# Optimization experiments

Measured on AMD Instinct MI355X. Metric: run time of the kernel, lower is better.

## Reference

```python
import jax, jax.numpy as jnp
import numpy as np

B, L, H, N = 8, 2048, 512, 64  # batch, seq_len, d_model, SSM state size


def setup_inputs() -> dict:
    key = jax.random.key(0)
    ks = jax.random.split(key, 10)
    x = jax.random.normal(ks[0], (B, L, H), jnp.float32)
    # S4D-style parameters (diagonal SSM, S4D-Lin init)
    log_dt = jnp.log(1e-3) + jax.random.uniform(ks[1], (H,), jnp.float32) * (jnp.log(1e-1) - jnp.log(1e-3))
    A_re = -0.5 * jnp.ones((H, N), jnp.float32)
    A_im = jnp.tile(np.pi * jnp.arange(N, dtype=np.float32), (H, 1))
    C_re = jax.random.normal(ks[2], (H, N), jnp.float32) * (0.5 ** 0.5)
    C_im = jax.random.normal(ks[3], (H, N), jnp.float32) * (0.5 ** 0.5)
    D_skip = jax.random.normal(ks[4], (H,), jnp.float32)
    # S4 output linear (GLU): d_model -> 2*d_model, then gated
    W_out = jax.random.normal(ks[5], (2 * H, H), jnp.float32) / np.sqrt(H)
    b_out = jnp.zeros((2 * H,), jnp.float32)
    # LayerNorms
    g1 = jnp.ones((H,), jnp.float32); beta1 = jnp.zeros((H,), jnp.float32)
    g2 = jnp.ones((H,), jnp.float32); beta2 = jnp.zeros((H,), jnp.float32)
    # 1x1 conv FFN (kernel_size=1 => pointwise linear), d_ff = d_model
    W1 = jax.random.normal(ks[6], (H, H), jnp.float32) / np.sqrt(H)
    bc1 = jnp.zeros((H,), jnp.float32)
    W2 = jax.random.normal(ks[7], (H, H), jnp.float32) / np.sqrt(H)
    bc2 = jnp.zeros((H,), jnp.float32)
    return dict(x=x, log_dt=log_dt, A_re=A_re, A_im=A_im, C_re=C_re, C_im=C_im,
                D_skip=D_skip, W_out=W_out, b_out=b_out, g1=g1, beta1=beta1,
                g2=g2, beta2=beta2, W1=W1, bc1=bc1, W2=W2, bc2=bc2)


def _layer_norm(x, g, b):
    mu = jnp.mean(x, axis=-1, keepdims=True)
    var = jnp.mean((x - mu) ** 2, axis=-1, keepdims=True)
    return (x - mu) / jnp.sqrt(var + 1e-5) * g + b


def _s4(x, log_dt, A_re, A_im, C_re, C_im, D_skip, W_out, b_out):
    # x: (B, L, H) channels-last (transposed=False)
    Lx = x.shape[1]
    dt = jnp.exp(log_dt)                       # (H,)
    A = A_re + 1j * A_im                       # (H, N) diagonal state matrix
    dtA = A * dt[:, None]
    # ZOH discretization of C: Ct = C * (exp(dt*A) - 1) / A
    Ct = (C_re + 1j * C_im) * ((jnp.exp(dtA) - 1.0) / A)
    # Vandermonde kernel: K[h, l] = 2 Re sum_n Ct[h,n] exp(dt*A[h,n]*l)
    l = jnp.arange(Lx, dtype=jnp.float32)
    K = 2.0 * jnp.real(jnp.einsum('hn,hnl->hl', Ct, jnp.exp(dtA[:, :, None] * l)))
    # FFT long convolution (linear conv via zero-padded circular conv)
    u = jnp.swapaxes(x, 1, 2)                  # (B, H, L)
    n = 2 * Lx
    y = jnp.fft.irfft(jnp.fft.rfft(u, n) * jnp.fft.rfft(K, n)[None], n)[..., :Lx]
    y = y + D_skip[None, :, None] * u          # skip connection D*u
    y = jax.nn.gelu(y)                         # S4 default activation
    # output linear + GLU (S4 default postact)
    z = jnp.einsum('bhl,fh->bfl', y, W_out) + b_out[None, :, None]
    a, g = jnp.split(z, 2, axis=1)
    y = a * jax.nn.sigmoid(g)
    return jnp.swapaxes(y, 1, 2)               # (B, L, H)


def reference(x, log_dt, A_re, A_im, C_re, C_im, D_skip, W_out, b_out,
              g1, beta1, g2, beta2, W1, bc1, W2, bc2):
    new_x = _s4(x, log_dt, A_re, A_im, C_re, C_im, D_skip, W_out, b_out)
    x = x + new_x
    x = _layer_norm(x, g1, beta1)
    # FFN via 1x1 convs (pointwise linears); dropout is identity in eval
    y = jax.nn.relu(jnp.einsum('blh,fh->blf', x, W1) + bc1)
    y = jnp.einsum('blf,hf->blh', y, W2) + bc2
    return _layer_norm(x + y, g2, beta2)
```

## Files before the change

### kernel.cpp

```cpp
#include <hip/hip_runtime.h>
#include <cstddef>
#include <cstdint>

#define B_DIM 8
#define L_DIM 2048
#define H_DIM 512
#define N_DIM 64
#define HN (H_DIM * N_DIM)
#define BLH (B_DIM * L_DIM * H_DIM)
#define M_DIM (B_DIM * L_DIM)

typedef unsigned short u16;
typedef short bf16x8 __attribute__((ext_vector_type(8)));
typedef float floatx4 __attribute__((ext_vector_type(4)));

__device__ __forceinline__ float sigmoidf_(float v) {
    return 1.0f / (1.0f + __expf(-v));
}

__device__ __forceinline__ float gelu_tanh_(float x) {
    float x3 = x * x * x;
    float z = 0.7978845608028654f * fmaf(0.044715f, x3, x);
    float e = __expf(-2.0f * fabsf(z));
    float th = (1.0f - e) / (1.0f + e);
    th = copysignf(th, z);
    return 0.5f * x * (1.0f + th);
}

__device__ __forceinline__ u16 f2b(float f) {
    unsigned u = __float_as_uint(f);
    unsigned r = (u + 0x7fffu + ((u >> 16) & 1u)) >> 16;
    return (u16)r;
}
__device__ __forceinline__ float b2f(u16 u) {
    return __uint_as_float(((unsigned)u) << 16);
}
__device__ __forceinline__ void unpack2(unsigned u, float& a, float& b) {
    a = __uint_as_float(u << 16);
    b = __uint_as_float(u & 0xffff0000u);
}
__device__ __forceinline__ unsigned pack2(float a, float b) {
    return (unsigned)f2b(a) | ((unsigned)f2b(b) << 16);
}

__device__ __forceinline__ void csq(float& r, float& i) {
    float nr = r * r - i * i;
    i = 2.0f * r * i;
    r = nr;
}

__global__ __launch_bounds__(256) void cast_kernel(
    const float* __restrict__ src, u16* __restrict__ dst)
{
    int i = blockIdx.x * 256 + threadIdx.x;
    float4 v = *(const float4*)(src + (size_t)i * 4);
    uint2 p;
    p.x = pack2(v.x, v.y);
    p.y = pack2(v.z, v.w);
    *(uint2*)(dst + (size_t)i * 4) = p;
}

__global__ __launch_bounds__(256) void precompute_kernel(
    const float* __restrict__ log_dt, const float* __restrict__ A_re,
    const float* __restrict__ A_im, const float* __restrict__ C_re,
    const float* __restrict__ C_im, float* __restrict__ P)
{
    int i = blockIdx.x * 256 + threadIdx.x;
    if (i >= HN) return;
    int h = i >> 6;
    float dt = expf(log_dt[h]);
    float Ar = A_re[i], Ai = A_im[i];
    float ar = dt * Ar, ai = dt * Ai;
    float e = expf(ar);
    float wr = e * cosf(ai);
    float wi = e * sinf(ai);
    float em1r = wr - 1.0f, em1i = wi;
    float inv = 1.0f / fmaf(Ar, Ar, Ai * Ai);
    float qr = fmaf(em1r, Ar, em1i * Ai) * inv;
    float qi = fmaf(em1i, Ar, -(em1r * Ai)) * inv;
    float Cr = C_re[i], Ci = C_im[i];
    float ctr = Cr * qr - Ci * qi;
    float cti = Cr * qi + Ci * qr;
    P[i]          = wr;
    P[HN + i]     = wi;
    P[2 * HN + i] = 2.0f * ctr;
    P[3 * HN + i] = 2.0f * cti;
}

__global__ __launch_bounds__(256) void ktab_kernel(
    const float* __restrict__ P, float* __restrict__ Ktab)
{
    int wv = threadIdx.x >> 6, lane = threadIdx.x & 63;
    int h = blockIdx.x * 4 + wv;
    int pidx = (h << 6) + lane;
    float wr = P[pidx], wi = P[HN + pidx];
    float c2r = P[2 * HN + pidx], c2i = P[3 * HN + pidx];
    float pr = 1.0f, pi = 0.0f;
    for (int tau = 0; tau < 64; ++tau) {
        float term = c2r * pr - c2i * pi;
        #pragma unroll
        for (int m = 32; m > 0; m >>= 1) term += __shfl_xor(term, m, 64);
        if (lane == 0) Ktab[(h << 6) + tau] = term;
        float nr = pr * wr - pi * wi, ni = pr * wi + pi * wr;
        pr = nr; pi = ni;
    }
}

__global__ __launch_bounds__(256) void toepfill_kernel(
    const float* __restrict__ Ktab, u16* __restrict__ Toep_bf)
{
    int idx = blockIdx.x * 256 + threadIdx.x;
    int h = idx >> 12;
    int rem = idx & 4095;
    int tt = rem >> 6, j = rem & 63;
    u16 v = 0;
    if (j <= tt) v = f2b(Ktab[(h << 6) + (tt - j)]);
    Toep_bf[idx] = v;
}

__global__ __launch_bounds__(256) void xtrans_kernel(
    const float* __restrict__ x, u16* __restrict__ XT)
{
    __shared__ float tile[32][33];
    int b  = blockIdx.z;
    int l0 = blockIdx.x * 32;
    int h0 = blockIdx.y * 32;
    int tx = threadIdx.x & 31;
    int ty = threadIdx.x >> 5;
    #pragma unroll
    for (int r = 0; r < 4; ++r)
        tile[ty + r * 8][tx] = x[((size_t)b * L_DIM + l0 + ty + r * 8) * H_DIM + h0 + tx];
    __syncthreads();
    #pragma unroll
    for (int r = 0; r < 4; ++r)
        XT[((size_t)b * H_DIM + h0 + ty + r * 8) * L_DIM + l0 + tx] = f2b(tile[tx][ty + r * 8]);
}

__global__ __launch_bounds__(256) void ssm_chunk_kernel(
    const u16* __restrict__ XT, const float* __restrict__ P,
    const u16* __restrict__ Toep_bf, const float* __restrict__ D_skip,
    u16* __restrict__ YT)
{
    __shared__ u16 U[128 * 72];
    __shared__ u16 S[128 * 136];
    __shared__ u16 EVT[13312];
    u16* E  = EVT;
    u16* Tp = EVT;
    u16* V  = EVT + 4608;

    const int h    = blockIdx.x;
    const int b0   = blockIdx.y * 4;
    const int t    = threadIdx.x;
    const int lane = t & 63;
    const int wv   = t >> 6;
    const int lm   = lane & 15, lq = lane >> 4;

    const int pidx = (h << 6) + lane;
    const float wr  = P[pidx],          wi  = P[HN + pidx];
    const float c2r = P[2 * HN + pidx], c2i = P[3 * HN + pidx];

    #pragma unroll
    for (int r = 0; r < 4; ++r) {
        int idx = t + r * 256;
        int row = idx >> 3, ch = idx & 7;
        const u16* gp = XT + (((size_t)(b0 + (row >> 5)) * H_DIM + h) << 11)
                           + ((row & 31) << 6) + (ch << 3);
        *(uint4*)&U[row * 72 + ch * 8] = *(const uint4*)gp;
    }

    float bwr, bwi;
    {
        float g16r = wr, g16i = wi;
        csq(g16r, g16i); csq(g16r, g16i); csq(g16r, g16i); csq(g16r, g16i);
        if (wv == 0)      { bwr = 1.0f; bwi = 0.0f; }
        else if (wv == 1) { bwr = g16r; bwi = g16i; }
        else if (wv == 2) { bwr = g16r; bwi = g16i; csq(bwr, bwi); }
        else {
            float g32r = g16r, g32i = g16i; csq(g32r, g32i);
            bwr = g32r * g16r - g32i * g16i;
            bwi = g32r * g16i + g32i * g16r;
        }
    }

    {
        float pr = bwr, pi = bwi;
        #pragma unroll
        for (int jk = 0; jk < 16; ++jk) {
            int k = (wv << 4) + jk;
            int j = 63 - k;
            E[(2 * lane) * 72 + j]     = f2b(pr);
            E[(2 * lane + 1) * 72 + j] = f2b(pi);
            float nr = pr * wr - pi * wi, ni = pr * wi + pi * wr;
            pr = nr; pi = ni;
        }
    }
    __syncthreads();

    {
        const int wm = wv >> 1, wn = wv & 1;
        floatx4 acc[4][4] = {};
        #pragma unroll
        for (int ks = 0; ks < 2; ++ks) {
            bf16x8 af[4], bfv[4];
            #pragma unroll
            for (int i = 0; i < 4; ++i)
                af[i] = *(const bf16x8*)&E[(wm * 64 + i * 16 + lm) * 72 + ks * 32 + lq * 8];
            #pragma unroll
            for (int j = 0; j < 4; ++j)
                bfv[j] = *(const bf16x8*)&U[(wn * 64 + j * 16 + lm) * 72 + ks * 32 + lq * 8];
            #pragma unroll
            for (int i = 0; i < 4; ++i) {
                #pragma unroll
                for (int j = 0; j < 4; ++j)
                    acc[i][j] = __builtin_amdgcn_mfma_f32_16x16x32_bf16(af[i], bfv[j], acc[i][j], 0, 0, 0);
            }
        }
        #pragma unroll
        for (int i = 0; i < 4; ++i) {
            #pragma unroll
            for (int j = 0; j < 4; ++j) {
                int ncol = wn * 64 + j * 16 + lm;
                int m0   = wm * 64 + i * 16 + lq * 4;
                u16 pk[4];
                #pragma unroll
                for (int r = 0; r < 4; ++r) pk[r] = f2b(acc[i][j][r]);
                *(uint2*)&S[ncol * 136 + m0] = *(uint2*)pk;
            }
        }
    }
    __syncthreads();

    {
        float pr = bwr, pi = bwi;
        {
            float nr = pr * wr - pi * wi, ni = pr * wi + pi * wr;
            pr = nr; pi = ni;
        }
        #pragma unroll
        for (int jk = 1; jk <= 16; ++jk) {
            int tr = (wv << 4) + jk - 1;
            float qr = c2r * pr - c2i * pi;
            float qi = c2r * pi + c2i * pr;
            V[tr * 136 + 2 * lane]     = f2b(qr);
            V[tr * 136 + 2 * lane + 1] = f2b(-qi);
            float nr = pr * wr - pi * wi, ni = pr * wi + pi * wr;
            pr = nr; pi = ni;
        }
        #pragma unroll
        for (int r = 0; r < 2; ++r) {
            int idx = t + r * 256;
            int row = idx >> 3, ch = idx & 7;
            *(uint4*)&Tp[row * 72 + ch * 8] =
                *(const uint4*)&Toep_bf[((size_t)h << 12) + (row << 6) + (ch << 3)];
        }
        float wTr = wr, wTi = wi;
        csq(wTr, wTi); csq(wTr, wTi); csq(wTr, wTi);
        csq(wTr, wTi); csq(wTr, wTi); csq(wTr, wTi);
        float Sr = 0.0f, Si = 0.0f;
        const int n2 = lane * 2;
        for (int c = 0; c < 32; ++c) {
            int base = (wv * 32 + c) * 136 + n2;
            unsigned lv = *(unsigned*)&S[base];
            float lr, li;
            unpack2(lv, lr, li);
            *(unsigned*)&S[base] = pack2(Sr, Si);
            float nSr = wTr * Sr - wTi * Si + lr;
            Si = wTr * Si + wTi * Sr + li;
            Sr = nSr;
        }
    }
    __syncthreads();

    {
        const float Dh = D_skip[h];
        floatx4 acc[4][2] = {};
        #pragma unroll
        for (int ks = 0; ks < 6; ++ks) {
            bf16x8 af[4], bfv[2];
            if (ks < 2) {
                #pragma unroll
                for (int i = 0; i < 4; ++i)
                    af[i] = *(const bf16x8*)&Tp[(i * 16 + lm) * 72 + ks * 32 + lq * 8];
                #pragma unroll
                for (int j = 0; j < 2; ++j)
                    bfv[j] = *(const bf16x8*)&U[(wv * 32 + j * 16 + lm) * 72 + ks * 32 + lq * 8];
            } else {
                #pragma unroll
                for (int i = 0; i < 4; ++i)
                    af[i] = *(const bf16x8*)&V[(i * 16 + lm) * 136 + (ks - 2) * 32 + lq * 8];
                #pragma unroll
                for (int j = 0; j < 2; ++j)
                    bfv[j] = *(const bf16x8*)&S[(wv * 32 + j * 16 + lm) * 136 + (ks - 2) * 32 + lq * 8];
            }
            #pragma unroll
            for (int i = 0; i < 4; ++i) {
                #pragma unroll
                for (int j = 0; j < 2; ++j)
                    acc[i][j] = __builtin_amdgcn_mfma_f32_16x16x32_bf16(af[i], bfv[j], acc[i][j], 0, 0, 0);
            }
        }
        #pragma unroll
        for (int j = 0; j < 2; ++j) {
            int ncol = wv * 32 + j * 16 + lm;
            int bloc = ncol >> 5, c = ncol & 31;
            size_t gbase = (((size_t)(b0 + bloc) * H_DIM + h) << 11) + (c << 6);
            #pragma unroll
            for (int i = 0; i < 4; ++i) {
                int t0 = i * 16 + lq * 4;
                u16 upk[4];
                *(uint2*)upk = *(const uint2*)&U[ncol * 72 + t0];
                u16 opk[4];
                #pragma unroll
                for (int r = 0; r < 4; ++r) {
                    float uvv = b2f(upk[r]);
                    float yv = gelu_tanh_(fmaf(Dh, uvv, acc[i][j][r]));
                    opk[r] = f2b(yv);
                }
                *(uint2*)&YT[gbase + t0] = *(uint2*)opk;
            }
        }
    }
}

__global__ __launch_bounds__(256) void ytrans_kernel(
    const u16* __restrict__ YT, u16* __restrict__ Y)
{
    __shared__ u16 tile[32][33];
    int b  = blockIdx.z;
    int l0 = blockIdx.x * 32;
    int h0 = blockIdx.y * 32;
    int tx = threadIdx.x & 31;
    int ty = threadIdx.x >> 5;
    #pragma unroll
    for (int r = 0; r < 4; ++r)
        tile[ty + r * 8][tx] = YT[((size_t)b * H_DIM + h0 + ty + r * 8) * L_DIM + l0 + tx];
    __syncthreads();
    #pragma unroll
    for (int r = 0; r < 4; ++r)
        Y[((size_t)b * L_DIM + l0 + ty + r * 8) * H_DIM + h0 + tx] = tile[tx][ty + r * 8];
}

__device__ __forceinline__ void stage_tile_128x32(
    const u16* __restrict__ g, u16* lds, int row0, int k0)
{
    const int t = threadIdx.x;
    #pragma unroll
    for (int r = 0; r < 2; ++r) {
        int row = (t >> 2) + r * 64;
        int col = (t & 3) * 8;
        const u16* gp = g + (size_t)(row0 + row) * 512 + k0 + col;
        __builtin_amdgcn_global_load_lds(
            (const __attribute__((address_space(1))) unsigned int*)gp,
            (__attribute__((address_space(3))) unsigned int*)(lds + (size_t)t * 8 + (size_t)r * 2048),
            16, 0, 0);
    }
}

__global__ __launch_bounds__(256) void gemm1_glu_kernel(
    const u16* __restrict__ A, const u16* __restrict__ Wo,
    const float* __restrict__ bo, const float* __restrict__ x,
    u16* __restrict__ out)
{
    __shared__ u16 As[2][128 * 32];
    __shared__ u16 Ba[2][128 * 32];
    __shared__ u16 Bg[2][128 * 32];
    const int t    = threadIdx.x;
    const int lane = t & 63;
    const int wv   = t >> 6;
    const int wm   = wv >> 1, wn = wv & 1;
    const int lm   = lane & 15, lq = lane >> 4;
    const int m0   = blockIdx.x * 128, n0 = blockIdx.y * 128;
    floatx4 accA[4][4] = {};
    floatx4 accG[4][4] = {};

    stage_tile_128x32(A, As[0], m0, 0);
    stage_tile_128x32(Wo, Ba[0], n0, 0);
    stage_tile_128x32(Wo, Bg[0], 512 + n0, 0);
    __syncthreads();

    int cur = 0;
    for (int k0 = 32; k0 < 512; k0 += 32) {
        const int nx = cur ^ 1;
        stage_tile_128x32(A, As[nx], m0, k0);
        stage_tile_128x32(Wo, Ba[nx], n0, k0);
        stage_tile_128x32(Wo, Bg[nx], 512 + n0, k0);

        bf16x8 af[4], ba[4], bg[4];
        #pragma unroll
        for (int i = 0; i < 4; ++i)
            af[i] = *(const bf16x8*)&As[cur][(wm * 64 + i * 16 + lm) * 32 + lq * 8];
        #pragma unroll
        for (int j = 0; j < 4; ++j) {
            ba[j] = *(const bf16x8*)&Ba[cur][(wn * 64 + j * 16 + lm) * 32 + lq * 8];
            bg[j] = *(const bf16x8*)&Bg[cur][(wn * 64 + j * 16 + lm) * 32 + lq * 8];
        }
        #pragma unroll
        for (int i = 0; i < 4; ++i) {
            #pragma unroll
            for (int j = 0; j < 4; ++j) {
                accA[i][j] = __builtin_amdgcn_mfma_f32_16x16x32_bf16(af[i], ba[j], accA[i][j], 0, 0, 0);
                accG[i][j] = __builtin_amdgcn_mfma_f32_16x16x32_bf16(af[i], bg[j], accG[i][j], 0, 0, 0);
            }
        }
        __syncthreads();
        cur = nx;
    }
    {
        bf16x8 af[4], ba[4], bg[4];
        #pragma unroll
        for (int i = 0; i < 4; ++i)
            af[i] = *(const bf16x8*)&As[cur][(wm * 64 + i * 16 + lm) * 32 + lq * 8];
        #pragma unroll
        for (int j = 0; j < 4; ++j) {
            ba[j] = *(const bf16x8*)&Ba[cur][(wn * 64 + j * 16 + lm) * 32 + lq * 8];
            bg[j] = *(const bf16x8*)&Bg[cur][(wn * 64 + j * 16 + lm) * 32 + lq * 8];
        }
        #pragma unroll
        for (int i = 0; i < 4; ++i) {
            #pragma unroll
            for (int j = 0; j < 4; ++j) {
                accA[i][j] = __builtin_amdgcn_mfma_f32_16x16x32_bf16(af[i], ba[j], accA[i][j], 0, 0, 0);
                accG[i][j] = __builtin_amdgcn_mfma_f32_16x16x32_bf16(af[i], bg[j], accG[i][j], 0, 0, 0);
            }
        }
    }
    #pragma unroll
    for (int j = 0; j < 4; ++j) {
        int n = n0 + wn * 64 + j * 16 + lm;
        float bav = bo[n], bgv = bo[512 + n];
        #pragma unroll
        for (int i = 0; i < 4; ++i) {
            #pragma unroll
            for (int r = 0; r < 4; ++r) {
                int m = m0 + wm * 64 + i * 16 + lq * 4 + r;
                float av = accA[i][j][r] + bav;
                float gv = accG[i][j][r] + bgv;
                float xv = x[(size_t)m * 512 + n];
                out[(size_t)m * 512 + n] = f2b(fmaf(av, sigmoidf_(gv), xv));
            }
        }
    }
}

template<int EPI>
__global__ __launch_bounds__(256) void gemm_bt_bf_kernel(
    const u16* __restrict__ A, const u16* __restrict__ Bw,
    const float* __restrict__ bias, u16* __restrict__ C)
{
    __shared__ u16 As[2][128 * 32];
    __shared__ u16 Bs[2][128 * 32];
    const int t    = threadIdx.x;
    const int lane = t & 63;
    const int wv   = t >> 6;
    const int wm   = wv >> 1, wn = wv & 1;
    const int lm   = lane & 15, lq = lane >> 4;
    const int m0   = blockIdx.x * 128, n0 = blockIdx.y * 128;
    floatx4 acc[4][4] = {};

    stage_tile_128x32(A, As[0], m0, 0);
    stage_tile_128x32(Bw, Bs[0], n0, 0);
    __syncthreads();

    int cur = 0;
    for (int k0 = 32; k0 < 512; k0 += 32) {
        const int nx = cur ^ 1;
        stage_tile_128x32(A, As[nx], m0, k0);
        stage_tile_128x32(Bw, Bs[nx], n0, k0);

        bf16x8 af[4], bfr[4];
        #pragma unroll
        for (int i = 0; i < 4; ++i)
            af[i] = *(const bf16x8*)&As[cur][(wm * 64 + i * 16 + lm) * 32 + lq * 8];
        #pragma unroll
        for (int j = 0; j < 4; ++j)
            bfr[j] = *(const bf16x8*)&Bs[cur][(wn * 64 + j * 16 + lm) * 32 + lq * 8];
        #pragma unroll
        for (int i = 0; i < 4; ++i) {
            #pragma unroll
            for (int j = 0; j < 4; ++j)
                acc[i][j] = __builtin_amdgcn_mfma_f32_16x16x32_bf16(af[i], bfr[j], acc[i][j], 0, 0, 0);
        }
        __syncthreads();
        cur = nx;
    }
    {
        bf16x8 af[4], bfr[4];
        #pragma unroll
        for (int i = 0; i < 4; ++i)
            af[i] = *(const bf16x8*)&As[cur][(wm * 64 + i * 16 + lm) * 32 + lq * 8];
        #pragma unroll
        for (int j = 0; j < 4; ++j)
            bfr[j] = *(const bf16x8*)&Bs[cur][(wn * 64 + j * 16 + lm) * 32 + lq * 8];
        #pragma unroll
        for (int i = 0; i < 4; ++i) {
            #pragma unroll
            for (int j = 0; j < 4; ++j)
                acc[i][j] = __builtin_amdgcn_mfma_f32_16x16x32_bf16(af[i], bfr[j], acc[i][j], 0, 0, 0);
        }
    }
    #pragma unroll
    for (int j = 0; j < 4; ++j) {
        int n = n0 + wn * 64 + j * 16 + lm;
        float bv = bias[n];
        #pragma unroll
        for (int i = 0; i < 4; ++i) {
            #pragma unroll
            for (int r = 0; r < 4; ++r) {
                int m = m0 + wm * 64 + i * 16 + lq * 4 + r;
                float v = acc[i][j][r] + bv;
                if (EPI == 1) v = fmaxf(v, 0.0f);
                C[(size_t)m * 512 + n] = f2b(v);
            }
        }
    }
}

template<bool HASRES, bool F32OUT>
__global__ __launch_bounds__(256) void ln_bf_kernel(
    const u16* __restrict__ in, const u16* __restrict__ res,
    const float* __restrict__ gamma, const float* __restrict__ beta,
    u16* __restrict__ outb, float* __restrict__ outf)
{
    int w    = threadIdx.x >> 6;
    int lane = threadIdx.x & 63;
    size_t row  = (size_t)blockIdx.x * 4 + w;
    size_t base = row * 512 + lane * 8;
    uint4 raw = *(const uint4*)(in + base);
    float v[8];
    unpack2(raw.x, v[0], v[1]); unpack2(raw.y, v[2], v[3]);
    unpack2(raw.z, v[4], v[5]); unpack2(raw.w, v[6], v[7]);
    if (HASRES) {
        uint4 rr = *(const uint4*)(res + base);
        float rv[8];
        unpack2(rr.x, rv[0], rv[1]); unpack2(rr.y, rv[2], rv[3]);
        unpack2(rr.z, rv[4], rv[5]); unpack2(rr.w, rv[6], rv[7]);
        #pragma unroll
        for (int i = 0; i < 8; ++i) v[i] += rv[i];
    }
    float s = 0.0f, sq = 0.0f;
    #pragma unroll
    for (int i = 0; i < 8; ++i) { s += v[i]; sq = fmaf(v[i], v[i], sq); }
    #pragma unroll
    for (int m = 32; m > 0; m >>= 1) {
        s  += __shfl_xor(s, m, 64);
        sq += __shfl_xor(sq, m, 64);
    }
    float mu  = s * (1.0f / 512.0f);
    float var = sq * (1.0f / 512.0f) - mu * mu;
    float rs  = rsqrtf(var + 1e-5f);
    float g[8], bt[8];
    *(float4*)&g[0]  = *(const float4*)(gamma + lane * 8);
    *(float4*)&g[4]  = *(const float4*)(gamma + lane * 8 + 4);
    *(float4*)&bt[0] = *(const float4*)(beta + lane * 8);
    *(float4*)&bt[4] = *(const float4*)(beta + lane * 8 + 4);
    float o[8];
    #pragma unroll
    for (int i = 0; i < 8; ++i)
        o[i] = fmaf((v[i] - mu) * rs, g[i], bt[i]);
    if (F32OUT) {
        *(float4*)(outf + base)     = *(float4*)&o[0];
        *(float4*)(outf + base + 4) = *(float4*)&o[4];
    } else {
        uint4 p;
        p.x = pack2(o[0], o[1]); p.y = pack2(o[2], o[3]);
        p.z = pack2(o[4], o[5]); p.w = pack2(o[6], o[7]);
        *(uint4*)(outb + base) = p;
    }
}

extern "C" void kernel_launch(void* const* d_in, const int* in_sizes, int n_in,
                              void* d_out, int out_size, void* d_ws, size_t ws_size,
                              hipStream_t stream)
{
    (void)in_sizes; (void)n_in; (void)out_size; (void)ws_size;
    const float* x      = (const float*)d_in[0];
    const float* log_dt = (const float*)d_in[1];
    const float* A_re   = (const float*)d_in[2];
    const float* A_im   = (const float*)d_in[3];
    const float* C_re   = (const float*)d_in[4];
    const float* C_im   = (const float*)d_in[5];
    const float* D_skip = (const float*)d_in[6];
    const float* W_out  = (const float*)d_in[7];
    const float* b_out  = (const float*)d_in[8];
    const float* g1     = (const float*)d_in[9];
    const float* beta1  = (const float*)d_in[10];
    const float* g2     = (const float*)d_in[11];
    const float* beta2  = (const float*)d_in[12];
    const float* W1     = (const float*)d_in[13];
    const float* bc1    = (const float*)d_in[14];
    const float* W2     = (const float*)d_in[15];
    const float* bc2    = (const float*)d_in[16];
    float* out = (float*)d_out;

    char*  wsb    = (char*)d_ws;
    float* P      = (float*)wsb;
    float* Ktab   = (float*)(wsb + 4 * HN * 4);
    u16*   Toep   = (u16*)(wsb + 4 * HN * 4 + 512 * 64 * 4);
    u16*   Wobf   = Toep + 512 * 4096;
    u16*   W1bf   = Wobf + 1024 * 512;
    u16*   W2bf   = W1bf + 512 * 512;
    u16*   r1     = W2bf + 512 * 512;
    u16*   r2     = r1 + BLH;
    u16*   r3     = r2 + BLH;

    cast_kernel<<<512, 256, 0, stream>>>(W_out, Wobf);
    cast_kernel<<<256, 256, 0, stream>>>(W1, W1bf);
    cast_kernel<<<256, 256, 0, stream>>>(W2, W2bf);
    precompute_kernel<<<HN / 256, 256, 0, stream>>>(log_dt, A_re, A_im, C_re, C_im, P);
    ktab_kernel<<<128, 256, 0, stream>>>(P, Ktab);
    toepfill_kernel<<<8192, 256, 0, stream>>>(Ktab, Toep);
    xtrans_kernel<<<dim3(L_DIM / 32, H_DIM / 32, B_DIM), 256, 0, stream>>>(x, r1);
    ssm_chunk_kernel<<<dim3(H_DIM, 2), 256, 0, stream>>>(r1, P, Toep, D_skip, r2);
    ytrans_kernel<<<dim3(L_DIM / 32, H_DIM / 32, B_DIM), 256, 0, stream>>>(r2, r3);
    gemm1_glu_kernel<<<dim3(M_DIM / 128, 4), 256, 0, stream>>>(r3, Wobf, b_out, x, r2);
    ln_bf_kernel<false, false><<<M_DIM / 4, 256, 0, stream>>>(r2, nullptr, g1, beta1, r1, nullptr);
    gemm_bt_bf_kernel<1><<<dim3(M_DIM / 128, 4), 256, 0, stream>>>(r1, W1bf, bc1, r3);
    gemm_bt_bf_kernel<0><<<dim3(M_DIM / 128, 4), 256, 0, stream>>>(r3, W2bf, bc2, r2);
    ln_bf_kernel<true, true><<<M_DIM / 4, 256, 0, stream>>>(r2, r1, g2, beta2, nullptr, out);
}
```

Baseline: 253.8 us.

## Use 512-thread GEMM blocks with XOR-swizzled LDS tiles

The three bf16 GEMM kernels now run 8 waves per block instead of 4. Each wave computes a 64x32 sub-tile instead of 64x64, which halves accumulator registers per wave and roughly doubles the waves available to hide latency. Tile staging changes to one 16-byte global-to-LDS load per thread, with an XOR swizzle on the source column. Fragment reads apply the matching swizzle to avoid LDS bank conflicts. In exchange, the A fragments are reloaded by twice as many waves, which adds LDS read traffic per MFMA.

```diff
diff --git a/kernel.cpp b/kernel.cpp
--- a/kernel.cpp
+++ b/kernel.cpp
@@ -340,23 +340,20 @@
         Y[((size_t)b * L_DIM + l0 + ty + r * 8) * H_DIM + h0 + tx] = tile[tx][ty + r * 8];
 }
 
-__device__ __forceinline__ void stage_tile_128x32(
+__device__ __forceinline__ void stage_tile_512(
     const u16* __restrict__ g, u16* lds, int row0, int k0)
 {
     const int t = threadIdx.x;
-    #pragma unroll
-    for (int r = 0; r < 2; ++r) {
-        int row = (t >> 2) + r * 64;
-        int col = (t & 3) * 8;
-        const u16* gp = g + (size_t)(row0 + row) * 512 + k0 + col;
-        __builtin_amdgcn_global_load_lds(
-            (const __attribute__((address_space(1))) unsigned int*)gp,
-            (__attribute__((address_space(3))) unsigned int*)(lds + (size_t)t * 8 + (size_t)r * 2048),
-            16, 0, 0);
-    }
-}
-
-__global__ __launch_bounds__(256) void gemm1_glu_kernel(
+    const int row  = t >> 2;
+    const int csrc = (t & 3) ^ ((t >> 3) & 3);
+    const u16* gp = g + (size_t)(row0 + row) * 512 + k0 + csrc * 8;
+    __builtin_amdgcn_global_load_lds(
+        (const __attribute__((address_space(1))) unsigned int*)gp,
+        (__attribute__((address_space(3))) unsigned int*)(lds + (size_t)t * 8),
+        16, 0, 0);
+}
+
+__global__ __launch_bounds__(512) void gemm1_glu_kernel(
     const u16* __restrict__ A, const u16* __restrict__ Wo,
     const float* __restrict__ bo, const float* __restrict__ x,
     u16* __restrict__ out)
@@ -367,37 +364,38 @@
     const int t    = threadIdx.x;
     const int lane = t & 63;
     const int wv   = t >> 6;
-    const int wm   = wv >> 1, wn = wv & 1;
+    const int wm   = wv >> 2, wn = wv & 3;
     const int lm   = lane & 15, lq = lane >> 4;
+    const int sw   = (lq ^ ((lm >> 1) & 3)) * 8;
     const int m0   = blockIdx.x * 128, n0 = blockIdx.y * 128;
-    floatx4 accA[4][4] = {};
-    floatx4 accG[4][4] = {};
-
-    stage_tile_128x32(A, As[0], m0, 0);
-    stage_tile_128x32(Wo, Ba[0], n0, 0);
-    stage_tile_128x32(Wo, Bg[0], 512 + n0, 0);
+    floatx4 accA[4][2] = {};
+    floatx4 accG[4][2] = {};
+
+    stage_tile_512(A, As[0], m0, 0);
+    stage_tile_512(Wo, Ba[0], n0, 0);
+    stage_tile_512(Wo, Bg[0], 512 + n0, 0);
     __syncthreads();
 
     int cur = 0;
     for (int k0 = 32; k0 < 512; k0 += 32) {
         const int nx = cur ^ 1;
-        stage_tile_128x32(A, As[nx], m0, k0);
-        stage_tile_128x32(Wo, Ba[nx], n0, k0);
-        stage_tile_128x32(Wo, Bg[nx], 512 + n0, k0);
-
-        bf16x8 af[4], ba[4], bg[4];
+        stage_tile_512(A, As[nx], m0, k0);
+        stage_tile_512(Wo, Ba[nx], n0, k0);
+        stage_tile_512(Wo, Bg[nx], 512 + n0, k0);
+
+        bf16x8 af[4], ba[2], bg[2];
         #pragma unroll
         for (int i = 0; i < 4; ++i)
-            af[i] = *(const bf16x8*)&As[cur][(wm * 64 + i * 16 + lm) * 32 + lq * 8];
-        #pragma unroll
-        for (int j = 0; j < 4; ++j) {
-            ba[j] = *(const bf16x8*)&Ba[cur][(wn * 64 + j * 16 + lm) * 32 + lq * 8];
-            bg[j] = *(const bf16x8*)&Bg[cur][(wn * 64 + j * 16 + lm) * 32 + lq * 8];
+            af[i] = *(const bf16x8*)&As[cur][(wm * 64 + i * 16 + lm) * 32 + sw];
+        #pragma unroll
+        for (int j = 0; j < 2; ++j) {
+            ba[j] = *(const bf16x8*)&Ba[cur][(wn * 32 + j * 16 + lm) * 32 + sw];
+            bg[j] = *(const bf16x8*)&Bg[cur][(wn * 32 + j * 16 + lm) * 32 + sw];
         }
         #pragma unroll
         for (int i = 0; i < 4; ++i) {
             #pragma unroll
-            for (int j = 0; j < 4; ++j) {
+            for (int j = 0; j < 2; ++j) {
                 accA[i][j] = __builtin_amdgcn_mfma_f32_16x16x32_bf16(af[i], ba[j], accA[i][j], 0, 0, 0);
                 accG[i][j] = __builtin_amdgcn_mfma_f32_16x16x32_bf16(af[i], bg[j], accG[i][j], 0, 0, 0);
             }
@@ -406,27 +404,27 @@
         cur = nx;
     }
     {
-        bf16x8 af[4], ba[4], bg[4];
+        bf16x8 af[4], ba[2], bg[2];
         #pragma unroll
         for (int i = 0; i < 4; ++i)
-            af[i] = *(const bf16x8*)&As[cur][(wm * 64 + i * 16 + lm) * 32 + lq * 8];
-        #pragma unroll
-        for (int j = 0; j < 4; ++j) {
-            ba[j] = *(const bf16x8*)&Ba[cur][(wn * 64 + j * 16 + lm) * 32 + lq * 8];
-            bg[j] = *(const bf16x8*)&Bg[cur][(wn * 64 + j * 16 + lm) * 32 + lq * 8];
+            af[i] = *(const bf16x8*)&As[cur][(wm * 64 + i * 16 + lm) * 32 + sw];
+        #pragma unroll
+        for (int j = 0; j < 2; ++j) {
+            ba[j] = *(const bf16x8*)&Ba[cur][(wn * 32 + j * 16 + lm) * 32 + sw];
+            bg[j] = *(const bf16x8*)&Bg[cur][(wn * 32 + j * 16 + lm) * 32 + sw];
         }
         #pragma unroll
         for (int i = 0; i < 4; ++i) {
             #pragma unroll
-            for (int j = 0; j < 4; ++j) {
+            for (int j = 0; j < 2; ++j) {
                 accA[i][j] = __builtin_amdgcn_mfma_f32_16x16x32_bf16(af[i], ba[j], accA[i][j], 0, 0, 0);
                 accG[i][j] = __builtin_amdgcn_mfma_f32_16x16x32_bf16(af[i], bg[j], accG[i][j], 0, 0, 0);
             }
         }
     }
     #pragma unroll
-    for (int j = 0; j < 4; ++j) {
-        int n = n0 + wn * 64 + j * 16 + lm;
+    for (int j = 0; j < 2; ++j) {
+        int n = n0 + wn * 32 + j * 16 + lm;
         float bav = bo[n], bgv = bo[512 + n];
         #pragma unroll
         for (int i = 0; i < 4; ++i) {
@@ -443,7 +441,7 @@
 }
 
 template<int EPI>
-__global__ __launch_bounds__(256) void gemm_bt_bf_kernel(
+__global__ __launch_bounds__(512) void gemm_bt_bf_kernel(
     const u16* __restrict__ A, const u16* __restrict__ Bw,
     const float* __restrict__ bias, u16* __restrict__ C)
 {
@@ -452,55 +450,56 @@
     const int t    = threadIdx.x;
     const int lane = t & 63;
     const int wv   = t >> 6;
-    const int wm   = wv >> 1, wn = wv & 1;
+    const int wm   = wv >> 2, wn = wv & 3;
     const int lm   = lane & 15, lq = lane >> 4;
+    const int sw   = (lq ^ ((lm >> 1) & 3)) * 8;
     const int m0   = blockIdx.x * 128, n0 = blockIdx.y * 128;
-    floatx4 acc[4][4] = {};
-
-    stage_tile_128x32(A, As[0], m0, 0);
-    stage_tile_128x32(Bw, Bs[0], n0, 0);
+    floatx4 acc[4][2] = {};
+
+    stage_tile_512(A, As[0], m0, 0);
+    stage_tile_512(Bw, Bs[0], n0, 0);
     __syncthreads();
 
     int cur = 0;
     for (int k0 = 32; k0 < 512; k0 += 32) {
         const int nx = cur ^ 1;
-        stage_tile_128x32(A, As[nx], m0, k0);
-        stage_tile_128x32(Bw, Bs[nx], n0, k0);
-
-        bf16x8 af[4], bfr[4];
+        stage_tile_512(A, As[nx], m0, k0);
+        stage_tile_512(Bw, Bs[nx], n0, k0);
+
+        bf16x8 af[4], bfr[2];
         #pragma unroll
         for (int i = 0; i < 4; ++i)
-            af[i] = *(const bf16x8*)&As[cur][(wm * 64 + i * 16 + lm) * 32 + lq * 8];
-        #pragma unroll
-        for (int j = 0; j < 4; ++j)
-            bfr[j] = *(const bf16x8*)&Bs[cur][(wn * 64 + j * 16 + lm) * 32 + lq * 8];
+            af[i] = *(const bf16x8*)&As[cur][(wm * 64 + i * 16 + lm) * 32 + sw];
+        #pragma unroll
+        for (int j = 0; j < 2; ++j)
+            bfr[j] = *(const bf16x8*)&Bs[cur][(wn * 32 + j * 16 + lm) * 32 + sw];
         #pragma unroll
         for (int i = 0; i < 4; ++i) {
             #pragma unroll
-            for (int j = 0; j < 4; ++j)
+            for (int j = 0; j < 2; ++j)
                 acc[i][j] = __builtin_amdgcn_mfma_f32_16x16x32_bf16(af[i], bfr[j], acc[i][j], 0, 0, 0);
         }
         __syncthreads();
         cur = nx;
     }
     {
-        bf16x8 af[4], bfr[4];
+        bf16x8 af[4], bfr[2];
         #pragma unroll
         for (int i = 0; i < 4; ++i)
-            af[i] = *(const bf16x8*)&As[cur][(wm * 64 + i * 16 + lm) * 32 + lq * 8];
-        #pragma unroll
-        for (int j = 0; j < 4; ++j)
-            bfr[j] = *(const bf16x8*)&Bs[cur][(wn * 64 + j * 16 + lm) * 32 + lq * 8];
+            af[i] = *(const bf16x8*)&As[cur][(wm * 64 + i * 16 + lm) * 32 + sw];
+        #pragma unroll
+        for (int j = 0; j < 2; ++j)
+            bfr[j] = *(const bf16x8*)&Bs[cur][(wn * 32 + j * 16 + lm) * 32 + sw];
         #pragma unroll
         for (int i = 0; i < 4; ++i) {
             #pragma unroll
-            for (int j = 0; j < 4; ++j)
+            for (int j = 0; j < 2; ++j)
                 acc[i][j] = __builtin_amdgcn_mfma_f32_16x16x32_bf16(af[i], bfr[j], acc[i][j], 0, 0, 0);
         }
     }
     #pragma unroll
-    for (int j = 0; j < 4; ++j) {
-        int n = n0 + wn * 64 + j * 16 + lm;
+    for (int j = 0; j < 2; ++j) {
+        int n = n0 + wn * 32 + j * 16 + lm;
         float bv = bias[n];
         #pragma unroll
         for (int i = 0; i < 4; ++i) {
@@ -612,9 +611,9 @@
     xtrans_kernel<<<dim3(L_DIM / 32, H_DIM / 32, B_DIM), 256, 0, stream>>>(x, r1);
     ssm_chunk_kernel<<<dim3(H_DIM, 2), 256, 0, stream>>>(r1, P, Toep, D_skip, r2);
     ytrans_kernel<<<dim3(L_DIM / 32, H_DIM / 32, B_DIM), 256, 0, stream>>>(r2, r3);
-    gemm1_glu_kernel<<<dim3(M_DIM / 128, 4), 256, 0, stream>>>(r3, Wobf, b_out, x, r2);
+    gemm1_glu_kernel<<<dim3(M_DIM / 128, 4), 512, 0, stream>>>(r3, Wobf, b_out, x, r2);
     ln_bf_kernel<false, false><<<M_DIM / 4, 256, 0, stream>>>(r2, nullptr, g1, beta1, r1, nullptr);
-    gemm_bt_bf_kernel<1><<<dim3(M_DIM / 128, 4), 256, 0, stream>>>(r1, W1bf, bc1, r3);
-    gemm_bt_bf_kernel<0><<<dim3(M_DIM / 128, 4), 256, 0, stream>>>(r3, W2bf, bc2, r2);
+    gemm_bt_bf_kernel<1><<<dim3(M_DIM / 128, 4), 512, 0, stream>>>(r1, W1bf, bc1, r3);
+    gemm_bt_bf_kernel<0><<<dim3(M_DIM / 128, 4), 512, 0, stream>>>(r3, W2bf, bc2, r2);
     ln_bf_kernel<true, true><<<M_DIM / 4, 256, 0, stream>>>(r2, r1, g2, beta2, nullptr, out);
 }
```

Result: no change. 250.6 us (-1.3%).
